# Kernel optimization log

Measured on AMD Instinct MI355X. Metric: run time of the kernel, lower is better.

The kernel has to match this reference:

```python
import jax, jax.numpy as jnp
import numpy as np

EPS = 1e-6
T_MAX = 0.999  # occlusion threshold used by compute_paths


def _dot(a, b):
    return jnp.sum(a * b, axis=-1)


def _mirror(p, v, n):
    # Reflect point p across plane through v with unit normal n.
    return p - 2.0 * _dot(p - v, n)[..., None] * n


def image_method(frm, to, mirror_v, mirror_n):
    """frm/to: [...,3]; mirror_v/mirror_n: [...,order,3] -> paths [...,order,3]."""
    order = mirror_v.shape[-2]
    images = []
    cur = frm
    for i in range(order):  # forward pass: successive images of TX
        cur = _mirror(cur, mirror_v[..., i, :], mirror_n[..., i, :])
        images.append(cur)
    paths = [None] * order
    nxt = to
    for i in range(order - 1, -1, -1):  # backward pass: intersect with planes
        img = images[i]
        v = mirror_v[..., i, :]
        n = mirror_n[..., i, :]
        d = nxt - img
        denom = _dot(d, n)
        t = _dot(v - img, n) / jnp.where(jnp.abs(denom) < EPS, EPS, denom)
        nxt = img + t[..., None] * d
        paths[i] = nxt
    return jnp.stack(paths, axis=-2)


def triangles_contain(tv, p):
    """tv: [...,3,3] triangle vertices, p: [...,3] point in same plane -> bool."""
    v0, v1, v2 = tv[..., 0, :], tv[..., 1, :], tv[..., 2, :]
    n0 = jnp.cross(p - v0, v1 - v0)
    n1 = jnp.cross(p - v1, v2 - v1)
    n2 = jnp.cross(p - v2, v0 - v2)
    d01, d12, d20 = _dot(n0, n1), _dot(n1, n2), _dot(n2, n0)
    pos = (d01 >= 0) & (d12 >= 0) & (d20 >= 0)
    neg = (d01 <= 0) & (d12 <= 0) & (d20 <= 0)
    return pos | neg


def same_side_of_mirrors(full_paths, mirror_v, mirror_n):
    """full_paths: [...,order+2,3]; consecutive vertices around each mirror on same side."""
    order = mirror_v.shape[-2]
    prev_v = full_paths[..., :order, :]
    next_v = full_paths[..., 2:, :]
    d_prev = _dot(prev_v - mirror_v, mirror_n)
    d_next = _dot(next_v - mirror_v, mirror_n)
    return d_prev * d_next >= 0


def rays_intersect_triangles(o, d, tv):
    """Moller-Trumbore. o,d: [...,3]; tv: broadcastable [...,3,3] -> (t, hit)."""
    v0, v1, v2 = tv[..., 0, :], tv[..., 1, :], tv[..., 2, :]
    e1 = v1 - v0
    e2 = v2 - v0
    h = jnp.cross(d, e2)
    a = _dot(e1, h)
    inv = 1.0 / jnp.where(jnp.abs(a) < EPS, 1.0, a)
    s = o - v0
    u = _dot(s, h) * inv
    q = jnp.cross(s, e1)
    v = _dot(d, q) * inv
    t = _dot(e2, q) * inv
    hit = (jnp.abs(a) > EPS) & (u >= 0.0) & (v >= 0.0) & (u + v <= 1.0) & (t > EPS)
    return t, hit


def compute_paths(transmitters, receivers, vertices, normals, triangles, path_candidates):
    P = path_candidates.shape[0]
    ntx = transmitters.shape[0]
    nrx = receivers.shape[0]
    all_tv = vertices[triangles]  # [T,3,3]

    frm = jnp.broadcast_to(transmitters[None, :, None, :], (P, ntx, nrx, 3))
    to = jnp.broadcast_to(receivers[None, None, :, :], (P, ntx, nrx, 3))

    pc_tv = all_tv[path_candidates]          # [P,order,3,3]
    mirror_v = pc_tv[..., 0, :]              # [P,order,3]
    mirror_n = normals[path_candidates]      # [P,order,3]
    tvb = pc_tv[:, None, None]               # [P,1,1,order,3,3]
    mvb = mirror_v[:, None, None]            # [P,1,1,order,3]
    mnb = mirror_n[:, None, None]

    paths = image_method(frm, to, mvb, mnb)  # [P,ntx,nrx,order,3]
    mask = jnp.all(triangles_contain(tvb, paths), axis=-1)

    full_paths = jnp.concatenate(
        (frm[..., None, :], paths, to[..., None, :]), axis=-2
    )  # [P,ntx,nrx,order+2,3]
    mask = mask & jnp.all(same_side_of_mirrors(full_paths, mvb, mnb), axis=-1)

    # Occlusion test: each of the order+1 segments vs every mesh triangle.
    ray_o = full_paths[..., :-1, None, :]       # [P,ntx,nrx,order+1,1,3]
    ray_d = jnp.diff(full_paths, axis=-2)[..., None, :]
    t, hit = rays_intersect_triangles(ray_o, ray_d, all_tv)  # [P,ntx,nrx,order+1,T]
    intersect = jnp.any((t < T_MAX) & hit, axis=(-1, -2))
    mask = mask & ~intersect

    # jit-friendly masking (original uses boolean fancy-indexing): zero-out invalid paths.
    return jnp.where(mask[..., None, None], full_paths, 0.0)


def setup_inputs() -> dict:
    key = jax.random.key(0)
    k1, k2, k3, k4 = jax.random.split(key, 4)
    V, T = 100, 128
    transmitters = 5.0 * jax.random.normal(k1, (1, 3), jnp.float32)
    receivers = 5.0 * jax.random.normal(k2, (1, 3), jnp.float32)
    vertices = jax.random.uniform(k3, (V, 3), jnp.float32, -10.0, 10.0)
    triangles = jax.random.randint(k4, (T, 3), 0, V, jnp.int32)
    tv = vertices[triangles]
    n = jnp.cross(tv[:, 1] - tv[:, 0], tv[:, 2] - tv[:, 0])
    normals = n / (jnp.linalg.norm(n, axis=-1, keepdims=True) + 1e-8)
    # generate_all_path_candidates(T, order=2): all ordered pairs (i,j), i != j
    idx = np.arange(T)
    ii, jj = np.meshgrid(idx, idx, indexing="ij")
    m = ii != jj
    path_candidates = jnp.asarray(np.stack([ii[m], jj[m]], axis=-1), jnp.int32)
    return {
        "transmitters": transmitters,
        "receivers": receivers,
        "vertices": vertices,
        "normals": normals,
        "triangles": triangles,
        "path_candidates": path_candidates,
        "order": 2,
    }


def reference(transmitters, receivers, vertices, normals, triangles, path_candidates, order):
    del order  # encoded in path_candidates.shape[-1]
    return compute_paths(transmitters, receivers, vertices, normals, triangles, path_candidates)
```

## Files before the change

### kernel.cpp

```cpp
#include <hip/hip_runtime.h>
#include <hip/hip_bf16.h>

#define EPS_F  1e-6f
#define TMAX_F 0.999f

struct F3 { float x, y, z; };

__device__ __forceinline__ F3 operator-(F3 a, F3 b){ return {a.x-b.x, a.y-b.y, a.z-b.z}; }
__device__ __forceinline__ F3 operator+(F3 a, F3 b){ return {a.x+b.x, a.y+b.y, a.z+b.z}; }
__device__ __forceinline__ F3 operator*(float s, F3 a){ return {s*a.x, s*a.y, s*a.z}; }
__device__ __forceinline__ float dot3(F3 a, F3 b){ return a.x*b.x + a.y*b.y + a.z*b.z; }
__device__ __forceinline__ F3 cross3(F3 a, F3 b){
  return { a.y*b.z - a.z*b.y, a.z*b.x - a.x*b.z, a.x*b.y - a.y*b.x };
}
__device__ __forceinline__ F3 ld3(const float* p){ return {p[0], p[1], p[2]}; }

__device__ __forceinline__ F3 mirror3(F3 p, F3 v, F3 n){
  float d = dot3(p - v, n);
  return p - (2.0f * d) * n;
}

__device__ __forceinline__ F3 plane_pt(F3 img, F3 v, F3 n, F3 nxt){
  F3 d = nxt - img;
  float den = dot3(d, n);
  float sd = (fabsf(den) < EPS_F) ? EPS_F : den;
  float t = dot3(v - img, n) / sd;
  return img + t * d;
}

__device__ __forceinline__ bool tri_contains(const float* tv9, F3 p){
  F3 a = ld3(tv9), b = ld3(tv9+3), c = ld3(tv9+6);
  F3 n0 = cross3(p - a, b - a);
  F3 n1 = cross3(p - b, c - b);
  F3 n2 = cross3(p - c, a - c);
  float d01 = dot3(n0, n1), d12 = dot3(n1, n2), d20 = dot3(n2, n0);
  bool pos = (d01 >= 0.f) & (d12 >= 0.f) & (d20 >= 0.f);
  bool neg = (d01 <= 0.f) & (d12 <= 0.f) & (d20 <= 0.f);
  return pos | neg;
}

__device__ __forceinline__ bool mt_block(F3 o, F3 d, const float* tv9){
  F3 a = ld3(tv9), b = ld3(tv9+3), c = ld3(tv9+6);
  F3 e1 = b - a, e2 = c - a;
  F3 h = cross3(d, e2);
  float det = dot3(e1, h);
  float safep = (fabsf(det) < EPS_F) ? 1.0f : det;
  float inv = 1.0f / safep;
  F3 s = o - a;
  float u = dot3(s, h) * inv;
  F3 q = cross3(s, e1);
  float v = dot3(d, q) * inv;
  float t = dot3(e2, q) * inv;
  bool hit = (fabsf(det) > EPS_F) & (u >= 0.f) & (v >= 0.f) & (u + v <= 1.f) & (t > EPS_F);
  return hit & (t < TMAX_F);
}

__global__ void __launch_bounds__(256)
paths_kernel(const float* __restrict__ txs, const float* __restrict__ rxs,
             const float* __restrict__ vertices, const float* __restrict__ normals,
             const int* __restrict__ triangles, const int* __restrict__ pc,
             int ntx, int nrx, int P, int T, float* __restrict__ out)
{
  extern __shared__ float smem[];
  float* tvS = smem;
  float* nS  = smem + T * 9;

  const int tid = threadIdx.x;
  for (int i = tid; i < T * 3; i += blockDim.x) {
    int vi = triangles[i];
    tvS[i*3+0] = vertices[vi*3+0];
    tvS[i*3+1] = vertices[vi*3+1];
    tvS[i*3+2] = vertices[vi*3+2];
    nS[i] = normals[i];
  }
  __syncthreads();

  const int lane  = tid & 63;
  const int waveInBlk = tid >> 6;
  const int wavesPerBlk = blockDim.x >> 6;
  const long long w = (long long)blockIdx.x * wavesPerBlk + waveInBlk;
  const long long total = (long long)P * ntx * nrx;
  if (w >= total) return;

  const int txrx = ntx * nrx;
  const int p  = (int)(w / txrx);
  const int r  = (int)(w % txrx);
  const int tx = r / nrx;
  const int rx = r % nrx;

  const F3 frm = ld3(txs + tx * 3);
  const F3 to  = ld3(rxs + rx * 3);

  const int t0 = pc[p*2 + 0];
  const int t1 = pc[p*2 + 1];

  const float* tv0 = tvS + t0 * 9;
  const float* tv1 = tvS + t1 * 9;
  const F3 v0 = ld3(tv0);
  const F3 n0 = ld3(nS + t0 * 3);
  const F3 v1 = ld3(tv1);
  const F3 n1 = ld3(nS + t1 * 3);

  const F3 img0 = mirror3(frm,  v0, n0);
  const F3 img1 = mirror3(img0, v1, n1);
  const F3 p1 = plane_pt(img1, v1, n1, to);
  const F3 p0 = plane_pt(img0, v0, n0, p1);

  bool mask = tri_contains(tv0, p0) & tri_contains(tv1, p1);

  float sp0 = dot3(frm - v0, n0) * dot3(p1 - v0, n0);
  float sp1 = dot3(p0  - v1, n1) * dot3(to - v1, n1);
  mask = mask & (sp0 >= 0.f) & (sp1 >= 0.f);

  if (mask) {
    F3 fp[4] = { frm, p0, p1, to };
    bool inter = false;
    #pragma unroll
    for (int seg = 0; seg < 3; ++seg) {
      F3 o = fp[seg];
      F3 d = fp[seg+1] - fp[seg];
      for (int tri = lane; tri < T; tri += 64) {
        inter |= mt_block(o, d, tvS + tri * 9);
      }
      if (__ballot(inter)) break;
    }
    mask = (__ballot(inter) == 0ULL);
  }

  if (lane == 0) {
    float4* o4 = reinterpret_cast<float4*>(out + (size_t)w * 12);
    if (mask) {
      o4[0] = make_float4(frm.x, frm.y, frm.z, p0.x);
      o4[1] = make_float4(p0.y,  p0.z,  p1.x,  p1.y);
      o4[2] = make_float4(p1.z,  to.x,  to.y,  to.z);
    } else {
      float4 z = make_float4(0.f, 0.f, 0.f, 0.f);
      o4[0] = z; o4[1] = z; o4[2] = z;
    }
  }
}

extern "C" void kernel_launch(void* const* d_in, const int* in_sizes, int n_in,
                              void* d_out, int out_size, void* d_ws, size_t ws_size,
                              hipStream_t stream) {
  const float* txs       = (const float*)d_in[0];
  const float* rxs       = (const float*)d_in[1];
  const float* vertices  = (const float*)d_in[2];
  const float* normals   = (const float*)d_in[3];
  const int*   triangles = (const int*)d_in[4];
  const int*   pc        = (const int*)d_in[5];

  const int ntx = in_sizes[0] / 3;
  const int nrx = in_sizes[1] / 3;
  const int T   = in_sizes[4] / 3;
  const int P   = in_sizes[5] / 2;

  float* out = (float*)d_out;

  const int block = 256;
  const int wavesPerBlk = block / 64;
  const long long totalWaves = (long long)P * ntx * nrx;
  const int grid = (int)((totalWaves + wavesPerBlk - 1) / wavesPerBlk);
  const size_t shmem = (size_t)T * 12 * sizeof(float);

  paths_kernel<<<grid, block, shmem, stream>>>(
      txs, rxs, vertices, normals, triangles, pc, ntx, nrx, P, T, out);
}
```

Baseline: 75.86 us.

## Compute one path candidate per lane and occlusion-test only valid candidates

Each lane now computes one candidate path's image-method geometry, instead of one wave per candidate. A ballot of the valid mask lets the whole wave occlusion-test only the surviving candidates, with their path points shared through LDS. This stops 64 lanes from redundantly running the cheap geometry and avoids launching waves for the many candidates that fail the mirror tests. In exchange, blocks shrink to 64 threads, and each block reloads the full triangle table into shared memory, which raises the per-block setup cost.

```diff
diff --git a/kernel.cpp b/kernel.cpp
--- a/kernel.cpp
+++ b/kernel.cpp
@@ -55,7 +55,7 @@
   return hit & (t < TMAX_F);
 }
 
-__global__ void __launch_bounds__(256)
+__global__ void __launch_bounds__(64)
 paths_kernel(const float* __restrict__ txs, const float* __restrict__ rxs,
              const float* __restrict__ vertices, const float* __restrict__ normals,
              const int* __restrict__ triangles, const int* __restrict__ pc,
@@ -63,10 +63,11 @@
 {
   extern __shared__ float smem[];
   float* tvS = smem;
-  float* nS  = smem + T * 9;
+  float* nS  = tvS + T * 9;
+  float* fpS = nS + T * 3;
 
-  const int tid = threadIdx.x;
-  for (int i = tid; i < T * 3; i += blockDim.x) {
+  const int lane = threadIdx.x;
+  for (int i = lane; i < T * 3; i += 64) {
     int vi = triangles[i];
     tvS[i*3+0] = vertices[vi*3+0];
     tvS[i*3+1] = vertices[vi*3+1];
@@ -75,16 +76,14 @@
   }
   __syncthreads();
 
-  const int lane  = tid & 63;
-  const int waveInBlk = tid >> 6;
-  const int wavesPerBlk = blockDim.x >> 6;
-  const long long w = (long long)blockIdx.x * wavesPerBlk + waveInBlk;
   const long long total = (long long)P * ntx * nrx;
-  if (w >= total) return;
+  const long long c = (long long)blockIdx.x * 64 + lane;
+  const bool valid = c < total;
+  const long long cc = valid ? c : 0;
 
   const int txrx = ntx * nrx;
-  const int p  = (int)(w / txrx);
-  const int r  = (int)(w % txrx);
+  const int p  = (int)(cc / txrx);
+  const int r  = (int)(cc % txrx);
   const int tx = r / nrx;
   const int rx = r % nrx;
 
@@ -94,11 +93,9 @@
   const int t0 = pc[p*2 + 0];
   const int t1 = pc[p*2 + 1];
 
-  const float* tv0 = tvS + t0 * 9;
-  const float* tv1 = tvS + t1 * 9;
-  const F3 v0 = ld3(tv0);
+  const F3 v0 = ld3(tvS + t0 * 9);
   const F3 n0 = ld3(nS + t0 * 3);
-  const F3 v1 = ld3(tv1);
+  const F3 v1 = ld3(tvS + t1 * 9);
   const F3 n1 = ld3(nS + t1 * 3);
 
   const F3 img0 = mirror3(frm,  v0, n0);
@@ -106,14 +103,25 @@
   const F3 p1 = plane_pt(img1, v1, n1, to);
   const F3 p0 = plane_pt(img0, v0, n0, p1);
 
-  bool mask = tri_contains(tv0, p0) & tri_contains(tv1, p1);
-
+  bool mask = tri_contains(tvS + t0 * 9, p0) & tri_contains(tvS + t1 * 9, p1);
   float sp0 = dot3(frm - v0, n0) * dot3(p1 - v0, n0);
   float sp1 = dot3(p0  - v1, n1) * dot3(to - v1, n1);
-  mask = mask & (sp0 >= 0.f) & (sp1 >= 0.f);
+  mask = mask & (sp0 >= 0.f) & (sp1 >= 0.f) & valid;
 
-  if (mask) {
-    F3 fp[4] = { frm, p0, p1, to };
+  float* myfp = fpS + lane * 12;
+  myfp[0]=frm.x; myfp[1]=frm.y; myfp[2]=frm.z;
+  myfp[3]=p0.x;  myfp[4]=p0.y;  myfp[5]=p0.z;
+  myfp[6]=p1.x;  myfp[7]=p1.y;  myfp[8]=p1.z;
+  myfp[9]=to.x;  myfp[10]=to.y; myfp[11]=to.z;
+  __syncthreads();
+
+  unsigned long long alive = __ballot(mask);
+  unsigned long long occl = 0ULL;
+  while (alive) {
+    const int s = __builtin_ctzll(alive);
+    alive &= alive - 1;
+    const float* sfp = fpS + s * 12;
+    F3 fp[4] = { ld3(sfp), ld3(sfp+3), ld3(sfp+6), ld3(sfp+9) };
     bool inter = false;
     #pragma unroll
     for (int seg = 0; seg < 3; ++seg) {
@@ -124,12 +132,14 @@
       }
       if (__ballot(inter)) break;
     }
-    mask = (__ballot(inter) == 0ULL);
+    if (__ballot(inter)) occl |= (1ULL << s);
   }
 
-  if (lane == 0) {
-    float4* o4 = reinterpret_cast<float4*>(out + (size_t)w * 12);
-    if (mask) {
+  const bool final_mask = mask && !((occl >> lane) & 1ULL);
+
+  if (valid) {
+    float4* o4 = reinterpret_cast<float4*>(out + (size_t)c * 12);
+    if (final_mask) {
       o4[0] = make_float4(frm.x, frm.y, frm.z, p0.x);
       o4[1] = make_float4(p0.y,  p0.z,  p1.x,  p1.y);
       o4[2] = make_float4(p1.z,  to.x,  to.y,  to.z);
@@ -157,12 +167,10 @@
 
   float* out = (float*)d_out;
 
-  const int block = 256;
-  const int wavesPerBlk = block / 64;
-  const long long totalWaves = (long long)P * ntx * nrx;
-  const int grid = (int)((totalWaves + wavesPerBlk - 1) / wavesPerBlk);
-  const size_t shmem = (size_t)T * 12 * sizeof(float);
+  const long long total = (long long)P * ntx * nrx;
+  const int grid = (int)((total + 63) / 64);
+  const size_t shmem = (size_t)(T * 12 + 64 * 12) * sizeof(float);
 
-  paths_kernel<<<grid, block, shmem, stream>>>(
+  paths_kernel<<<grid, 64, shmem, stream>>>(
       txs, rxs, vertices, normals, triangles, pc, ntx, nrx, P, T, out);
 }
```

After: 74.68 us. Within noise of the previous version (-1.5%).
